# Kernel optimization log

Measured on AMD Instinct MI355X. Metric: run time of the kernel, lower is better.

Reference implementation:

```python
import jax, jax.numpy as jnp
import numpy as np

V, E, H, L, S, B, FE = 50257, 768, 12, 4, 1024, 2, 4
HD = E // H
EPS = 1e-5


def setup_inputs() -> dict:
    key = jax.random.key(0)
    ks = jax.random.split(key, 16)
    def n(k, shape, scale=0.02):
        return jax.random.normal(k, shape, jnp.float32) * scale
    x = jax.random.randint(ks[0], (B, S), 0, V)
    mask = jnp.tril(jnp.ones((S, S), jnp.int32))[None, None]  # (1,1,S,S) causal
    return {
        "x": x,
        "mask": mask,
        "embed_W": n(ks[1], (V, E)),
        "pos_embed": n(ks[2], (1, S, E)),
        "fc_out_W": n(ks[3], (L, E, E)),
        "fc_out_b": jnp.zeros((L, E), jnp.float32),
        "gate_W": n(ks[4], (L, E, E)),
        "gate_b": jnp.zeros((L, E), jnp.float32),
        "ln1_g": jnp.ones((L, E), jnp.float32),
        "ln1_b": jnp.zeros((L, E), jnp.float32),
        "ln2_g": jnp.ones((L, E), jnp.float32),
        "ln2_b": jnp.zeros((L, E), jnp.float32),
        "ff1_W": n(ks[5], (L, E, FE * E)),
        "ff1_b": jnp.zeros((L, FE * E), jnp.float32),
        "ff2_W": n(ks[6], (L, FE * E, E)),
        "ff2_b": jnp.zeros((L, E), jnp.float32),
        "lnf_g": jnp.ones((E,), jnp.float32),
        "lnf_b": jnp.zeros((E,), jnp.float32),
        "head_W": n(ks[7], (E, V)),
    }


def _layernorm(y, g, b):
    m = jnp.mean(y, -1, keepdims=True)
    v = jnp.mean((y - m) ** 2, -1, keepdims=True)
    return (y - m) * jax.lax.rsqrt(v + EPS) * g + b


def reference(x, mask, embed_W, pos_embed, fc_out_W, fc_out_b, gate_W, gate_b,
              ln1_g, ln1_b, ln2_g, ln2_b, ff1_W, ff1_b, ff2_W, ff2_b,
              lnf_g, lnf_b, head_W):
    h = embed_W[x] + pos_embed[:, :x.shape[1], :]  # (B,S,E)
    scale = 1.0 / np.sqrt(HD)
    for i in range(L):
        # NOTE: source never applies the q/k/v Linear layers; heads are split directly.
        q = h.reshape(B, S, H, HD).transpose(0, 2, 1, 3)  # (B,H,S,HD)
        energy = jnp.einsum('bhqd,bhkd->bhqk', q, q)
        energy = jnp.where(mask == 0, jnp.float32(-1e20), energy)
        attn = jax.nn.softmax(energy * scale, axis=-1)
        o = jnp.einsum('bhqk,bhkd->bhqd', attn, q)
        o = o.transpose(0, 2, 1, 3).reshape(B, S, E)
        o = o @ fc_out_W[i] + fc_out_b[i]
        gate = jax.nn.sigmoid(jnp.mean(h, 1, keepdims=True) @ gate_W[i] + gate_b[i])
        h = _layernorm(gate * o + h, ln1_g[i], ln1_b[i])
        ff = jax.nn.gelu(h @ ff1_W[i] + ff1_b[i], approximate=False) @ ff2_W[i] + ff2_b[i]
        h = _layernorm(ff + h, ln2_g[i], ln2_b[i])
    h = _layernorm(h, lnf_g, lnf_b)
    logits = h @ head_W  # (B,S,V)
    return logits
```

## Files before the change

### kernel.cpp

```cpp
#include <hip/hip_runtime.h>
#include <hip/hip_bf16.h>

#define V 50257
#define E 768
#define NH 12
#define NL 4
#define SS 1024
#define BB 2
#define FEE 4
#define HD 64
#define EPSL 1e-5f
#define NPADH 50432

typedef __hip_bfloat16 bf16;
typedef __attribute__((ext_vector_type(8))) short short8;
typedef __attribute__((ext_vector_type(4))) float f32x4;
typedef __attribute__((ext_vector_type(4), aligned(4))) float f32x4a;

#define GLD_SRC(p) (const __attribute__((address_space(1))) void*)(p)
#define GLD_DST(p) (__attribute__((address_space(3))) void*)(p)

__global__ __launch_bounds__(256) void embed_kernel(const int* __restrict__ x, const float* __restrict__ eW,
                                                    const float* __restrict__ pos, float* __restrict__ h,
                                                    bf16* __restrict__ hb){
  size_t i = (size_t)blockIdx.x*256 + threadIdx.x;
  if (i >= (size_t)BB*SS*E) return;
  int e = (int)(i % E);
  size_t bs = i / E;
  int s = (int)(bs % SS);
  int tok = x[bs];
  float v = eW[(size_t)tok*E + e] + pos[(size_t)s*E + e];
  h[i] = v;
  hb[i] = __float2bfloat16(v);
}

__global__ __launch_bounds__(256) void cvt_attn(const bf16* __restrict__ hb, bf16* __restrict__ vT){
  __shared__ short t[64][65];
  int bid = blockIdx.x;
  int st = bid & 15, hh = (bid >> 4) % NH, b = bid / (16*NH);
  int s0 = st*64;
  int c = threadIdx.x & 63, rr = threadIdx.x >> 6;
  #pragma unroll
  for (int i = 0; i < 16; ++i){
    int r = rr*16 + i;
    t[r][c] = __builtin_bit_cast(short, hb[(size_t)(b*SS + s0 + r)*E + hh*HD + c]);
  }
  __syncthreads();
  #pragma unroll
  for (int i = 0; i < 16; ++i){
    int d = rr*16 + i;
    vT[(size_t)((b*NH + hh)*HD + d)*SS + s0 + c] = __builtin_bit_cast(bf16, t[c][d]);
  }
}

__global__ __launch_bounds__(256) void attn_mfma(const bf16* __restrict__ hb, const bf16* __restrict__ vT,
                                                 bf16* __restrict__ Ab){
  __shared__ short Qs[64*64];
  __shared__ short Ks[128*64];
  __shared__ short Vs[64*128];
  __shared__ short Ps[4][16*128];
  int tid = threadIdx.x, wave = tid >> 6, lane = tid & 63;
  int bid = blockIdx.x;
  int qt = 15 - (bid & 15);
  int hh = (bid >> 4) % NH, b = bid / (16*NH);
  int q0 = qt*64;
  int l15 = lane & 15, l4 = lane >> 4;
  int sw7 = l15 & 7;

  #pragma unroll
  for (int rnd = 0; rnd < 2; ++rnd){
    int o = rnd*256 + tid; int row = o >> 3; int cs = (((o & 7) ^ (row & 7))*8);
    __builtin_amdgcn_global_load_lds(GLD_SRC(hb + ((size_t)(b*SS + q0 + row)*E + hh*HD + cs)),
                                     GLD_DST(Qs + o*8), 16, 0, 0);
  }

  float mrun[4], lrun[4];
  #pragma unroll
  for (int j = 0; j < 4; ++j){ mrun[j] = -1e30f; lrun[j] = 0.f; }
  f32x4 acco[4] = {};

  int nkt = (qt >> 1) + 1;
  for (int kt = 0; kt < nkt; ++kt){
    int k0 = kt*128;
    __syncthreads();
    #pragma unroll
    for (int rnd = 0; rnd < 4; ++rnd){
      int o = rnd*256 + tid; int row = o >> 3; int cs = (((o & 7) ^ (row & 7))*8);
      __builtin_amdgcn_global_load_lds(GLD_SRC(hb + ((size_t)(b*SS + k0 + row)*E + hh*HD + cs)),
                                       GLD_DST(Ks + o*8), 16, 0, 0);
    }
    #pragma unroll
    for (int rnd = 0; rnd < 4; ++rnd){
      int o = rnd*256 + tid; int row = o >> 4; int cs = (((o & 15) ^ (row & 15))*8);
      __builtin_amdgcn_global_load_lds(GLD_SRC(vT + ((size_t)((b*NH + hh)*HD + row)*SS + k0 + cs)),
                                       GLD_DST(Vs + o*8), 16, 0, 0);
    }
    __syncthreads();

    f32x4 s[8] = {};
    __builtin_amdgcn_s_setprio(1);
    #pragma unroll
    for (int kk = 0; kk < 2; ++kk){
      int slot = kk*4 + l4;
      short8 af = *(const short8*)&Qs[(wave*16 + l15)*64 + ((slot ^ sw7)*8)];
      #pragma unroll
      for (int n = 0; n < 8; ++n){
        short8 bf8 = *(const short8*)&Ks[(n*16 + l15)*64 + ((slot ^ sw7)*8)];
        s[n] = __builtin_amdgcn_mfma_f32_16x16x32_bf16(af, bf8, s[n], 0, 0, 0);
      }
    }
    __builtin_amdgcn_s_setprio(0);

    bool diag = (kt == nkt - 1);
    #pragma unroll
    for (int j = 0; j < 4; ++j){
      int qg = q0 + wave*16 + l4*4 + j;
      float tmax = -1e30f;
      #pragma unroll
      for (int n = 0; n < 8; ++n){
        float v = s[n][j]*0.125f;
        if (diag && (k0 + n*16 + l15) > qg) v = -1e30f;
        s[n][j] = v; tmax = fmaxf(tmax, v);
      }
      tmax = fmaxf(tmax, __shfl_xor(tmax, 1, 64));
      tmax = fmaxf(tmax, __shfl_xor(tmax, 2, 64));
      tmax = fmaxf(tmax, __shfl_xor(tmax, 4, 64));
      tmax = fmaxf(tmax, __shfl_xor(tmax, 8, 64));
      float mnew = fmaxf(mrun[j], tmax);
      float alpha = __expf(mrun[j] - mnew);
      float rsum = 0.f;
      #pragma unroll
      for (int n = 0; n < 8; ++n){
        float p = __expf(s[n][j] - mnew);
        s[n][j] = p; rsum += p;
      }
      rsum += __shfl_xor(rsum, 1, 64);
      rsum += __shfl_xor(rsum, 2, 64);
      rsum += __shfl_xor(rsum, 4, 64);
      rsum += __shfl_xor(rsum, 8, 64);
      lrun[j] = lrun[j]*alpha + rsum;
      mrun[j] = mnew;
      #pragma unroll
      for (int n = 0; n < 4; ++n) acco[n][j] *= alpha;
      int prow = l4*4 + j;
      #pragma unroll
      for (int n = 0; n < 8; ++n){
        bf16 hv = __float2bfloat16(s[n][j]);
        int slot = (n*2 + (l15 >> 3)) ^ prow;
        Ps[wave][prow*128 + slot*8 + (l15 & 7)] = __builtin_bit_cast(short, hv);
      }
    }
    __syncthreads();

    __builtin_amdgcn_s_setprio(1);
    #pragma unroll
    for (int kk = 0; kk < 4; ++kk){
      int slot = kk*4 + l4;
      short8 pa = *(const short8*)&Ps[wave][l15*128 + ((slot ^ l15)*8)];
      #pragma unroll
      for (int n = 0; n < 4; ++n){
        short8 vb = *(const short8*)&Vs[(n*16 + l15)*128 + ((slot ^ l15)*8)];
        acco[n] = __builtin_amdgcn_mfma_f32_16x16x32_bf16(pa, vb, acco[n], 0, 0, 0);
      }
    }
    __builtin_amdgcn_s_setprio(0);
  }

  #pragma unroll
  for (int j = 0; j < 4; ++j){
    float inv = 1.f / lrun[j];
    int qg = q0 + wave*16 + l4*4 + j;
    #pragma unroll
    for (int n = 0; n < 4; ++n){
      Ab[(size_t)(b*SS + qg)*E + hh*HD + n*16 + l15] = __float2bfloat16(acco[n][j]*inv);
    }
  }
}

__global__ __launch_bounds__(256) void hmean1_kernel(const float* __restrict__ h, float* __restrict__ ph){
  int bid = blockIdx.x;
  int ec = bid % 3, tc = (bid/3) & 15, b = bid / 48;
  int e = ec*256 + threadIdx.x;
  float s = 0.f;
  #pragma unroll 8
  for (int t = tc*64; t < tc*64 + 64; ++t) s += h[((size_t)b*SS + t)*E + e];
  ph[((size_t)b*16 + tc)*E + e] = s;
}

__global__ __launch_bounds__(256) void gate1_kernel(const float* __restrict__ ph, const float* __restrict__ gW,
                                                    float* __restrict__ pg){
  int bid = blockIdx.x;
  int ec = bid % 3, kc = (bid/3) & 3, b = bid / 12;
  int nn = ec*256 + threadIdx.x;
  __shared__ float hms[192];
  if (threadIdx.x < 192){
    int k = kc*192 + threadIdx.x;
    float s = 0.f;
    #pragma unroll
    for (int tc = 0; tc < 16; ++tc) s += ph[((size_t)b*16 + tc)*E + k];
    hms[threadIdx.x] = s * (1.0f/SS);
  }
  __syncthreads();
  float acc = 0.f;
  #pragma unroll 8
  for (int j = 0; j < 192; ++j) acc += hms[j] * gW[(size_t)(kc*192 + j)*E + nn];
  pg[((size_t)b*4 + kc)*E + nn] = acc;
}

__global__ __launch_bounds__(256) void wcvt_kernel(const float* __restrict__ W, bf16* __restrict__ Wt,
                                                   int K, int N, int Npad){
  int l = blockIdx.z;
  W  += (size_t)l*K*N;
  Wt += (size_t)l*Npad*K;
  __shared__ float t[32][33];
  int n0 = blockIdx.x*32, k0 = blockIdx.y*32;
  int tx = threadIdx.x & 31, ty8 = threadIdx.x >> 5;
  #pragma unroll
  for (int i = 0; i < 4; ++i){
    int k = k0 + ty8 + i*8, n = n0 + tx;
    t[ty8 + i*8][tx] = (k < K && n < N) ? W[(size_t)k*N + n] : 0.f;
  }
  __syncthreads();
  #pragma unroll
  for (int i = 0; i < 4; ++i){
    int n = n0 + ty8 + i*8, k = k0 + tx;
    if (n < Npad && k < K) Wt[(size_t)n*K + k] = __float2bfloat16(t[tx][ty8 + i*8]);
  }
}

template<int EPI>
__global__ __launch_bounds__(256, 2) void mfma_gemm(const bf16* __restrict__ A, const bf16* __restrict__ Bt,
                                                    const float* __restrict__ bias, void* __restrict__ Cv,
                                                    int M, int N, int Kslice, int Ktot){
  __shared__ short As[2][128*64];
  __shared__ short Bs[2][128*64];
  int tid = threadIdx.x;
  int wave = tid >> 6, lane = tid & 63;
  int wr = wave >> 1, wc = wave & 1;
  int l15 = lane & 15, l4 = lane >> 4;
  int sw7 = l15 & 7;
  int n0 = blockIdx.x * 128, m0 = blockIdx.y * 128;
  size_t koff = (size_t)blockIdx.z * Kslice;
  f32x4 acc[4][4] = {};
  int srow = tid >> 3;
  int sj = tid & 7;
  const int nks = Kslice >> 6;

  #define STAGE128(bsel, kt) do {                                              \
    int kb = (kt)*64;                                                          \
    _Pragma("unroll")                                                          \
    for (int iss = 0; iss < 4; ++iss){                                         \
      int r = srow + iss*32;                                                   \
      int cs = ((sj ^ (r & 7))*8);                                             \
      __builtin_amdgcn_global_load_lds(GLD_SRC(A + (size_t)(m0 + r)*Ktot + koff + kb + cs),  \
                                       GLD_DST(&As[bsel][r*64 + sj*8]), 16, 0, 0);           \
      __builtin_amdgcn_global_load_lds(GLD_SRC(Bt + (size_t)(n0 + r)*Ktot + koff + kb + cs), \
                                       GLD_DST(&Bs[bsel][r*64 + sj*8]), 16, 0, 0);           \
    }                                                                          \
  } while(0)

  STAGE128(0, 0);
  for (int kt = 0; kt < nks; ++kt){
    int cur = kt & 1;
    if (kt + 1 < nks){
      STAGE128(cur ^ 1, kt + 1);
      asm volatile("s_waitcnt vmcnt(8)" ::: "memory");
    } else {
      asm volatile("s_waitcnt vmcnt(0)" ::: "memory");
    }
    __builtin_amdgcn_s_barrier();
    __builtin_amdgcn_sched_barrier(0);
    __builtin_amdgcn_s_setprio(1);
    #pragma unroll
    for (int kk = 0; kk < 2; ++kk){
      int slot = kk*4 + l4;
      short8 af[4], bfr[4];
      #pragma unroll
      for (int m = 0; m < 4; ++m)
        af[m] = *(const short8*)&As[cur][(wr*64 + m*16 + l15)*64 + ((slot ^ sw7)*8)];
      #pragma unroll
      for (int n = 0; n < 4; ++n)
        bfr[n] = *(const short8*)&Bs[cur][(wc*64 + n*16 + l15)*64 + ((slot ^ sw7)*8)];
      #pragma unroll
      for (int m = 0; m < 4; ++m)
        #pragma unroll
        for (int n = 0; n < 4; ++n)
          acc[m][n] = __builtin_amdgcn_mfma_f32_16x16x32_bf16(af[m], bfr[n], acc[m][n], 0, 0, 0);
    }
    __builtin_amdgcn_s_setprio(0);
    __builtin_amdgcn_s_barrier();
    __builtin_amdgcn_sched_barrier(0);
  }
  #undef STAGE128

  if (EPI == 3){
    int lrow = l4*4;
    #pragma unroll
    for (int m = 0; m < 4; ++m){
      int row = m0 + wr*64 + m*16 + lrow;
      #pragma unroll
      for (int n = 0; n < 4; ++n){
        int col = n0 + wc*64 + n*16 + l15;
        if (col >= N) continue;
        #pragma unroll
        for (int j = 0; j < 4; ++j){
          float v = acc[m][n][j] + bias[col];
          v = 0.5f*v*(1.0f + erff(v*0.70710678f));
          ((bf16*)Cv)[(size_t)(row + j)*N + col] = __float2bfloat16(v);
        }
      }
    }
  } else {
    __syncthreads();
    float* Cf = (float*)Cv + (size_t)blockIdx.z * M * N;
    float* sw = ((float*)&As[0][0]) + wave*1104;
    int rbase = m0 + wr*64;
    int c0w = n0 + wc*64;
    #pragma unroll
    for (int m = 0; m < 4; ++m){
      #pragma unroll
      for (int n = 0; n < 4; ++n)
        #pragma unroll
        for (int j = 0; j < 4; ++j)
          sw[(l4*4 + j)*68 + n*16 + l15] = acc[m][n][j];
      #pragma unroll
      for (int jj = 0; jj < 4; ++jj){
        int rl = jj*4 + l4;
        f32x4a v = *(const f32x4a*)&sw[rl*68 + l15*4];
        int row = rbase + m*16 + rl;
        int col = c0w + l15*4;
        if (col + 3 < N){
          *(f32x4a*)&Cf[(size_t)row*N + col] = v;
        } else {
          #pragma unroll
          for (int c = 0; c < 4; ++c) if (col + c < N) Cf[(size_t)row*N + col + c] = v[c];
        }
      }
    }
  }
}

__global__ __launch_bounds__(512, 2) void gemm256(const bf16* __restrict__ A, const bf16* __restrict__ Bt,
                                                  float* __restrict__ C, int M, int N, int K, int MT){
  __shared__ short As[2][256*64];
  __shared__ short Bs[2][256*64];
  int tid = threadIdx.x;
  int wave = tid >> 6, lane = tid & 63;
  int wr = wave >> 2, wc = wave & 3;
  int l15 = lane & 15, l4 = lane >> 4;
  int sw7 = l15 & 7;

  int lid = blockIdx.x;
  int cpx = gridDim.x >> 3;
  int wg = (lid & 7)*cpx + (lid >> 3);
  int m0 = (wg % MT)*256, n0 = (wg / MT)*256;

  int srow = tid >> 3;
  int sj = tid & 7;
  const int nks = K >> 6;

  #define STAGE256(bsel, kt) do {                                             \
    int kb = (kt)*64;                                                         \
    _Pragma("unroll")                                                         \
    for (int rnd = 0; rnd < 4; ++rnd){                                        \
      int r = rnd*64 + srow;                                                  \
      int cs = ((sj ^ (r & 7))*8);                                            \
      __builtin_amdgcn_global_load_lds(GLD_SRC(A + (size_t)(m0 + r)*K + kb + cs),   \
                                       GLD_DST(&As[bsel][r*64 + sj*8]), 16, 0, 0);  \
      __builtin_amdgcn_global_load_lds(GLD_SRC(Bt + (size_t)(n0 + r)*K + kb + cs),  \
                                       GLD_DST(&Bs[bsel][r*64 + sj*8]), 16, 0, 0);  \
    }                                                                         \
  } while(0)

  f32x4 acc[8][4] = {};
  STAGE256(0, 0);
  for (int kt = 0; kt < nks; ++kt){
    int cur = kt & 1;
    if (kt + 1 < nks){
      STAGE256(cur ^ 1, kt + 1);
      asm volatile("s_waitcnt vmcnt(8)" ::: "memory");
    } else {
      asm volatile("s_waitcnt vmcnt(0)" ::: "memory");
    }
    __builtin_amdgcn_s_barrier();
    __builtin_amdgcn_sched_barrier(0);
    __builtin_amdgcn_s_setprio(1);
    #pragma unroll
    for (int kk = 0; kk < 2; ++kk){
      int slot = kk*4 + l4;
      short8 af[8], bfr[4];
      #pragma unroll
      for (int m = 0; m < 8; ++m)
        af[m] = *(const short8*)&As[cur][(wr*128 + m*16 + l15)*64 + ((slot ^ sw7)*8)];
      #pragma unroll
      for (int n = 0; n < 4; ++n)
        bfr[n] = *(const short8*)&Bs[cur][(wc*64 + n*16 + l15)*64 + ((slot ^ sw7)*8)];
      #pragma unroll
      for (int m = 0; m < 8; ++m)
        #pragma unroll
        for (int n = 0; n < 4; ++n)
          acc[m][n] = __builtin_amdgcn_mfma_f32_16x16x32_bf16(af[m], bfr[n], acc[m][n], 0, 0, 0);
    }
    __builtin_amdgcn_s_setprio(0);
    __builtin_amdgcn_s_barrier();
    __builtin_amdgcn_sched_barrier(0);
  }
  #undef STAGE256

  __syncthreads();
  float* sw = ((float*)&As[0][0]) + wave*1104;
  int rbase = m0 + wr*128;
  int c0w = n0 + wc*64;
  #pragma unroll
  for (int m = 0; m < 8; ++m){
    #pragma unroll
    for (int n = 0; n < 4; ++n)
      #pragma unroll
      for (int j = 0; j < 4; ++j)
        sw[(l4*4 + j)*68 + n*16 + l15] = acc[m][n][j];
    #pragma unroll
    for (int jj = 0; jj < 4; ++jj){
      int rl = jj*4 + l4;
      f32x4a v = *(const f32x4a*)&sw[rl*68 + l15*4];
      int row = rbase + m*16 + rl;
      int col = c0w + l15*4;
      if (col + 3 < N){
        *(f32x4a*)&C[(size_t)row*N + col] = v;
      } else {
        #pragma unroll
        for (int c = 0; c < 4; ++c) if (col + c < N) C[(size_t)row*N + col + c] = v[c];
      }
    }
  }
}

__global__ __launch_bounds__(256) void ln_kernel(const float* __restrict__ parts, int np,
                                                 const float* __restrict__ bias,
                                                 const float* __restrict__ resid,
                                                 const float* __restrict__ pg, const float* __restrict__ gb,
                                                 const float* __restrict__ g, const float* __restrict__ bta,
                                                 float* __restrict__ out, bf16* __restrict__ outb){
  const size_t PS = (size_t)BB*SS*E;
  int row = blockIdx.x;
  int b = row >> 10;
  int tid = threadIdx.x;
  __shared__ float sred[4];
  float y[3];
  float lsum = 0.f;
  #pragma unroll
  for (int i = 0; i < 3; ++i){
    int e = tid + i*256;
    float v = bias ? bias[e] : 0.f;
    for (int p = 0; p < np; ++p) v += parts[(size_t)p*PS + (size_t)row*E + e];
    if (pg){
      float ga = pg[(size_t)(b*4+0)*E + e] + pg[(size_t)(b*4+1)*E + e]
               + pg[(size_t)(b*4+2)*E + e] + pg[(size_t)(b*4+3)*E + e] + gb[e];
      v *= 1.0f / (1.0f + __expf(-ga));
    }
    if (resid) v += resid[(size_t)row*E + e];
    y[i] = v; lsum += v;
  }
  for (int off = 32; off > 0; off >>= 1) lsum += __shfl_down(lsum, off, 64);
  int wid = tid >> 6, lane = tid & 63;
  if (lane == 0) sred[wid] = lsum;
  __syncthreads();
  float mean = (sred[0]+sred[1]+sred[2]+sred[3]) * (1.0f/E);
  __syncthreads();
  float lvar = 0.f;
  #pragma unroll
  for (int i = 0; i < 3; ++i){ float d = y[i]-mean; lvar += d*d; }
  for (int off = 32; off > 0; off >>= 1) lvar += __shfl_down(lvar, off, 64);
  if (lane == 0) sred[wid] = lvar;
  __syncthreads();
  float rstd = rsqrtf((sred[0]+sred[1]+sred[2]+sred[3]) * (1.0f/E) + EPSL);
  __syncthreads();
  #pragma unroll
  for (int i = 0; i < 3; ++i){
    int e = tid + i*256;
    float r = (y[i]-mean)*rstd*g[e] + bta[e];
    out[(size_t)row*E + e] = r;
    if (outb) outb[(size_t)row*E + e] = __float2bfloat16(r);
  }
}

extern "C" void kernel_launch(void* const* d_in, const int* in_sizes, int n_in,
                              void* d_out, int out_size, void* d_ws, size_t ws_size,
                              hipStream_t stream) {
  const int*   x      = (const int*)  d_in[0];
  const float* embedW = (const float*)d_in[2];
  const float* pos    = (const float*)d_in[3];
  const float* fcW    = (const float*)d_in[4];
  const float* fcB    = (const float*)d_in[5];
  const float* gW     = (const float*)d_in[6];
  const float* gB     = (const float*)d_in[7];
  const float* ln1g   = (const float*)d_in[8];
  const float* ln1b   = (const float*)d_in[9];
  const float* ln2g   = (const float*)d_in[10];
  const float* ln2b   = (const float*)d_in[11];
  const float* f1W    = (const float*)d_in[12];
  const float* f1B    = (const float*)d_in[13];
  const float* f2W    = (const float*)d_in[14];
  const float* f2B    = (const float*)d_in[15];
  const float* lnfg   = (const float*)d_in[16];
  const float* lnfb   = (const float*)d_in[17];
  const float* headW  = (const float*)d_in[18];
  float* out = (float*)d_out;

  const size_t BSE = (size_t)BB*SS*E;
  float* h    = (float*)d_ws;
  float* o    = h   + BSE;
  float* tmp  = o   + BSE;
  float* ph   = tmp + 2*BSE;
  float* pg   = ph  + (size_t)BB*16*E;
  bf16* abA   = (bf16*)(pg + (size_t)BB*4*E);
  bf16* abF   = abA + BSE;
  bf16* WfcT  = abF + BSE*FEE;
  bf16* Wf1T  = WfcT + (size_t)NL*E*E;
  bf16* Wf2T  = Wf1T + (size_t)NL*FEE*E*E;
  bf16* WheadT= Wf2T + (size_t)NL*FEE*E*E;
  bf16* hb    = (bf16*)o;
  bf16* vT    = hb + BSE;

  const int rows = BB*SS;

  embed_kernel<<<(int)((BSE + 255)/256), 256, 0, stream>>>(x, embedW, pos, h, hb);

  { dim3 g(E/32, E/32, NL);        wcvt_kernel<<<g, 256, 0, stream>>>(fcW, WfcT, E, E, E); }
  { dim3 g((FEE*E)/32, E/32, NL);  wcvt_kernel<<<g, 256, 0, stream>>>(f1W, Wf1T, E, FEE*E, FEE*E); }
  { dim3 g(E/32, (FEE*E)/32, NL);  wcvt_kernel<<<g, 256, 0, stream>>>(f2W, Wf2T, FEE*E, E, E); }
  { dim3 g(NPADH/32, E/32, 1);     wcvt_kernel<<<g, 256, 0, stream>>>(headW, WheadT, E, V, NPADH); }

  for (int l = 0; l < NL; ++l){
    size_t oEE = (size_t)l*E*E, oE = (size_t)l*E, oFb = (size_t)l*FEE*E;

    hmean1_kernel<<<BB*16*3, 256, 0, stream>>>(h, ph);
    gate1_kernel<<<BB*4*3, 256, 0, stream>>>(ph, gW + oEE, pg);

    cvt_attn<<<BB*NH*16, 256, 0, stream>>>(hb, vT);
    attn_mfma<<<BB*NH*16, 256, 0, stream>>>(hb, vT, abA);

    { dim3 g(E/128, rows/128, 2);
      mfma_gemm<0><<<g, 256, 0, stream>>>(abA, WfcT + oEE, nullptr, tmp, rows, E, E/2, E); }

    ln_kernel<<<rows, 256, 0, stream>>>(tmp, 2, fcB + oE, h, pg, gB + oE,
                                        ln1g + oE, ln1b + oE, h, abA);

    { dim3 g((FEE*E)/128, rows/128, 1);
      mfma_gemm<3><<<g, 256, 0, stream>>>(abA, Wf1T + (size_t)l*FEE*E*E, f1B + oFb, abF, rows, FEE*E, E, E); }

    { dim3 g(E/128, rows/128, 2);
      mfma_gemm<0><<<g, 256, 0, stream>>>(abF, Wf2T + (size_t)l*FEE*E*E, nullptr, tmp, rows, E, FEE*E/2, FEE*E); }

    ln_kernel<<<rows, 256, 0, stream>>>(tmp, 2, f2B + oE, h, nullptr, nullptr,
                                        ln2g + oE, ln2b + oE, h, hb);
  }

  ln_kernel<<<rows, 256, 0, stream>>>(h, 1, nullptr, nullptr, nullptr, nullptr,
                                      lnfg, lnfb, tmp, abA);
  {
    gemm256<<<(rows/256)*(NPADH/256), 512, 0, stream>>>(abA, WheadT, out, rows, V, E, rows/256);
  }
}
```

Baseline: 1.017 ms.

## Double-buffer K/V tiles in attention with 64-wide key tiles

Rewrites the flash-attention loop to use 64-key tiles with double-buffered K and V shared-memory tiles. The next tile is prefetched with global_load_lds while the current one is computed, so only one waitcnt+barrier per iteration is needed. The per-wave P buffer is no longer followed by a block barrier, and launch bounds request 3 blocks per SM. The cost is more loop iterations with smaller MFMA batches, and the finer causal tiling also skips some masked work.

New measurement: 1.041 ms. 1.02x slower.

```diff
diff --git a/kernel.cpp b/kernel.cpp
--- a/kernel.cpp
+++ b/kernel.cpp
@@ -53,12 +53,12 @@
   }
 }
 
-__global__ __launch_bounds__(256) void attn_mfma(const bf16* __restrict__ hb, const bf16* __restrict__ vT,
-                                                 bf16* __restrict__ Ab){
+__global__ __launch_bounds__(256, 3) void attn_mfma(const bf16* __restrict__ hb, const bf16* __restrict__ vT,
+                                                    bf16* __restrict__ Ab){
   __shared__ short Qs[64*64];
-  __shared__ short Ks[128*64];
-  __shared__ short Vs[64*128];
-  __shared__ short Ps[4][16*128];
+  __shared__ short Ks[2][64*64];
+  __shared__ short Vs[2][64*64];
+  __shared__ short Ps[4][16*64];
   int tid = threadIdx.x, wave = tid >> 6, lane = tid & 63;
   int bid = blockIdx.x;
   int qt = 15 - (bid & 15);
@@ -67,45 +67,49 @@
   int l15 = lane & 15, l4 = lane >> 4;
   int sw7 = l15 & 7;
 
+  #define STG_KV(bsel, kt) do {                                                        \
+    int k0s = (kt)*64;                                                                 \
+    _Pragma("unroll")                                                                  \
+    for (int rnd = 0; rnd < 2; ++rnd){                                                 \
+      int o = rnd*256 + tid; int row = o >> 3; int cs = (((o & 7) ^ (row & 7))*8);     \
+      __builtin_amdgcn_global_load_lds(GLD_SRC(hb + ((size_t)(b*SS + k0s + row)*E + hh*HD + cs)), \
+                                       GLD_DST(&Ks[bsel][o*8]), 16, 0, 0);             \
+      __builtin_amdgcn_global_load_lds(GLD_SRC(vT + ((size_t)((b*NH + hh)*HD + row)*SS + k0s + cs)), \
+                                       GLD_DST(&Vs[bsel][o*8]), 16, 0, 0);             \
+    }                                                                                  \
+  } while(0)
+
   #pragma unroll
   for (int rnd = 0; rnd < 2; ++rnd){
     int o = rnd*256 + tid; int row = o >> 3; int cs = (((o & 7) ^ (row & 7))*8);
     __builtin_amdgcn_global_load_lds(GLD_SRC(hb + ((size_t)(b*SS + q0 + row)*E + hh*HD + cs)),
                                      GLD_DST(Qs + o*8), 16, 0, 0);
   }
+  STG_KV(0, 0);
+  asm volatile("s_waitcnt vmcnt(0)" ::: "memory");
+  __builtin_amdgcn_s_barrier();
+  __builtin_amdgcn_sched_barrier(0);
 
   float mrun[4], lrun[4];
   #pragma unroll
   for (int j = 0; j < 4; ++j){ mrun[j] = -1e30f; lrun[j] = 0.f; }
   f32x4 acco[4] = {};
 
-  int nkt = (qt >> 1) + 1;
+  int nkt = qt + 1;
   for (int kt = 0; kt < nkt; ++kt){
-    int k0 = kt*128;
-    __syncthreads();
-    #pragma unroll
-    for (int rnd = 0; rnd < 4; ++rnd){
-      int o = rnd*256 + tid; int row = o >> 3; int cs = (((o & 7) ^ (row & 7))*8);
-      __builtin_amdgcn_global_load_lds(GLD_SRC(hb + ((size_t)(b*SS + k0 + row)*E + hh*HD + cs)),
-                                       GLD_DST(Ks + o*8), 16, 0, 0);
-    }
-    #pragma unroll
-    for (int rnd = 0; rnd < 4; ++rnd){
-      int o = rnd*256 + tid; int row = o >> 4; int cs = (((o & 15) ^ (row & 15))*8);
-      __builtin_amdgcn_global_load_lds(GLD_SRC(vT + ((size_t)((b*NH + hh)*HD + row)*SS + k0 + cs)),
-                                       GLD_DST(Vs + o*8), 16, 0, 0);
-    }
-    __syncthreads();
-
-    f32x4 s[8] = {};
+    int k0 = kt*64;
+    int cur = kt & 1;
+    if (kt + 1 < nkt) STG_KV(cur ^ 1, kt + 1);
+
+    f32x4 s[4] = {};
     __builtin_amdgcn_s_setprio(1);
     #pragma unroll
     for (int kk = 0; kk < 2; ++kk){
       int slot = kk*4 + l4;
       short8 af = *(const short8*)&Qs[(wave*16 + l15)*64 + ((slot ^ sw7)*8)];
       #pragma unroll
-      for (int n = 0; n < 8; ++n){
-        short8 bf8 = *(const short8*)&Ks[(n*16 + l15)*64 + ((slot ^ sw7)*8)];
+      for (int n = 0; n < 4; ++n){
+        short8 bf8 = *(const short8*)&Ks[cur][(n*16 + l15)*64 + ((slot ^ sw7)*8)];
         s[n] = __builtin_amdgcn_mfma_f32_16x16x32_bf16(af, bf8, s[n], 0, 0, 0);
       }
     }
@@ -117,7 +121,7 @@
       int qg = q0 + wave*16 + l4*4 + j;
       float tmax = -1e30f;
       #pragma unroll
-      for (int n = 0; n < 8; ++n){
+      for (int n = 0; n < 4; ++n){
         float v = s[n][j]*0.125f;
         if (diag && (k0 + n*16 + l15) > qg) v = -1e30f;
         s[n][j] = v; tmax = fmaxf(tmax, v);
@@ -130,7 +134,7 @@
       float alpha = __expf(mrun[j] - mnew);
       float rsum = 0.f;
       #pragma unroll
-      for (int n = 0; n < 8; ++n){
+      for (int n = 0; n < 4; ++n){
         float p = __expf(s[n][j] - mnew);
         s[n][j] = p; rsum += p;
       }
@@ -144,27 +148,33 @@
       for (int n = 0; n < 4; ++n) acco[n][j] *= alpha;
       int prow = l4*4 + j;
       #pragma unroll
-      for (int n = 0; n < 8; ++n){
+      for (int n = 0; n < 4; ++n){
         bf16 hv = __float2bfloat16(s[n][j]);
-        int slot = (n*2 + (l15 >> 3)) ^ prow;
-        Ps[wave][prow*128 + slot*8 + (l15 & 7)] = __builtin_bit_cast(short, hv);
-      }
-    }
-    __syncthreads();
+        int slot = (n*2 + (l15 >> 3)) ^ (prow & 7);
+        Ps[wave][prow*64 + slot*8 + (l15 & 7)] = __builtin_bit_cast(short, hv);
+      }
+    }
 
     __builtin_amdgcn_s_setprio(1);
     #pragma unroll
-    for (int kk = 0; kk < 4; ++kk){
+    for (int kk = 0; kk < 2; ++kk){
       int slot = kk*4 + l4;
-      short8 pa = *(const short8*)&Ps[wave][l15*128 + ((slot ^ l15)*8)];
+      short8 pa = *(const short8*)&Ps[wave][l15*64 + ((slot ^ sw7)*8)];
       #pragma unroll
       for (int n = 0; n < 4; ++n){
-        short8 vb = *(const short8*)&Vs[(n*16 + l15)*128 + ((slot ^ l15)*8)];
+        short8 vb = *(const short8*)&Vs[cur][(n*16 + l15)*64 + ((slot ^ sw7)*8)];
         acco[n] = __builtin_amdgcn_mfma_f32_16x16x32_bf16(pa, vb, acco[n], 0, 0, 0);
       }
     }
     __builtin_amdgcn_s_setprio(0);
-  }
+
+    if (kt + 1 < nkt){
+      asm volatile("s_waitcnt vmcnt(0)" ::: "memory");
+      __builtin_amdgcn_s_barrier();
+      __builtin_amdgcn_sched_barrier(0);
+    }
+  }
+  #undef STG_KV
 
   #pragma unroll
   for (int j = 0; j < 4; ++j){
```
